# Performance work log

Hardware: AMD Instinct MI355X
Metric: run time of the kernel (lower is better)

## Reference

```python
import jax, jax.numpy as jnp
import numpy as np

C = 256          # in_channels == out_channels
L = 131072       # sequence length (multiple of BL)
BL = 64          # dilation == sliding-attention block length
CQ = C // 2      # q/k channels (r1=2)
CV = C // 2      # v channels (r2=2)
ALPHA = 1.0
EPS_IN = 1e-5    # InstanceNorm eps


def setup_inputs() -> dict:
    key = jax.random.key(0)
    ks = jax.random.split(key, 16)
    s = 0.05
    return {
        "x": jax.random.normal(ks[0], (1, C, L), jnp.float32),
        "f": jax.random.normal(ks[1], (1, C, L), jnp.float32),
        "mask": jnp.ones((1, 1, L), jnp.float32),
        # ConvFeedForward: Conv1d(C, C, 3, padding=BL, dilation=BL)
        "Wff": jax.random.normal(ks[2], (C, C, 3), jnp.float32) * s,
        "bff": jax.random.normal(ks[3], (C,), jnp.float32) * s,
        # AttLayer 1x1 convs
        "Wq": jax.random.normal(ks[4], (CQ, C), jnp.float32) * s,
        "bq": jax.random.normal(ks[5], (CQ,), jnp.float32) * s,
        "Wk": jax.random.normal(ks[6], (CQ, C), jnp.float32) * s,
        "bk": jax.random.normal(ks[7], (CQ,), jnp.float32) * s,
        "Wv": jax.random.normal(ks[8], (CV, C), jnp.float32) * s,
        "bv": jax.random.normal(ks[9], (CV,), jnp.float32) * s,
        "Wo": jax.random.normal(ks[10], (C, CV), jnp.float32) * s,
        "bo": jax.random.normal(ks[11], (C,), jnp.float32) * s,
        # AttModule.conv_1x1
        "Wc": jax.random.normal(ks[12], (C, C), jnp.float32) * s,
        "bc": jax.random.normal(ks[13], (C,), jnp.float32) * s,
    }


def _conv1x1(W, b, x):  # x: (B, Cin, L)
    return jnp.einsum('oc,bcl->bol', W, x) + b[None, :, None]


def _forward(x, f, mask, Wff, bff, Wq, bq, Wk, bk, Wv, bv, Wo, bo, Wc, bc):
    # --- ConvFeedForward: dilated conv + ReLU (same-length output) ---
    out = jax.lax.conv_general_dilated(
        x, Wff, window_strides=(1,), padding=[(BL, BL)], rhs_dilation=(BL,),
        dimension_numbers=('NCH', 'OIH', 'NCH')) + bff[None, :, None]
    out = jax.nn.relu(out)  # (1, C, L)

    # --- InstanceNorm1d (affine=False, biased var) ---
    mu = out.mean(axis=-1, keepdims=True)
    var = out.var(axis=-1, keepdims=True)
    xn = (out - mu) * jax.lax.rsqrt(var + EPS_IN)

    # --- AttLayer (sliding_att, decoder: value from f) ---
    q = _conv1x1(Wq, bq, xn)   # (1, CQ, L)
    k = _conv1x1(Wk, bk, xn)   # (1, CQ, L)
    v = _conv1x1(Wv, bv, f)    # (1, CV, L)

    nb = L // BL
    half = BL // 2
    pm = mask[:, 0:1, :]                         # (1,1,L) padding mask
    # pad halo of BL//2 zeros on each side of k, v, padding_mask
    kp = jnp.pad(k, ((0, 0), (0, 0), (half, half)))
    vp = jnp.pad(v, ((0, 0), (0, 0), (half, half)))
    mp = jnp.pad(pm, ((0, 0), (0, 0), (half, half)))
    # window index: block i sees [i*BL, i*BL + 2*BL) of the padded sequence
    idx = jnp.arange(nb)[:, None] * BL + jnp.arange(2 * BL)[None, :]  # (nb, 2BL)
    kw = kp[:, :, idx]   # (1, CQ, nb, 2BL)
    vw = vp[:, :, idx]   # (1, CV, nb, 2BL)
    mw = mp[:, 0, idx]   # (1, nb, 2BL)

    # window mask: query i attends keys [i, i+BL) within the 2BL window
    d = jnp.arange(2 * BL)[None, :] - jnp.arange(BL)[:, None]
    wm = ((d >= 0) & (d < BL)).astype(x.dtype)          # (BL, 2BL)
    fm = wm[None, None] * mw[:, :, None, :]             # (1, nb, BL, 2BL)

    qb = q.reshape(1, CQ, nb, BL)
    energy = jnp.einsum('bcnl,bcnm->bnlm', qb, kw) / np.sqrt(CQ).astype(x.dtype)
    att = jax.nn.softmax(energy + jnp.log(fm + 1e-6), axis=-1) * fm
    ov = jnp.einsum('bcnm,bnlm->bcnl', vw, att)         # (1, CV, nb, BL)
    oo = jnp.einsum('oc,bcnl->bonl', Wo, jax.nn.relu(ov)) + bo[None, :, None, None]
    att_out = oo.reshape(1, C, L) * pm                  # (1, C, L)

    # --- scaled residual + 1x1 conv + (dropout=identity) + masked residual ---
    h = ALPHA * att_out + out
    h = _conv1x1(Wc, bc, h)
    return (x + h) * mask


def reference(x, f, mask, Wff, bff, Wq, bq, Wk, bk, Wv, bv, Wo, bo, Wc, bc):
    return _forward(x, f, mask, Wff, bff, Wq, bq, Wk, bk, Wv, bv, Wo, bo, Wc, bc)
```

## Files before the change

### kernel.cpp

```cpp
#include <hip/hip_runtime.h>

#define L_LEN 131072
#define NB    2048
#define NT    1024

typedef unsigned short u16;
typedef __attribute__((ext_vector_type(4))) float f32x4;
typedef __attribute__((ext_vector_type(8))) short s16x8;
typedef __attribute__((ext_vector_type(4))) short s16x4;

#define WS_OUTT  0ull
#define WS_QT    67108864ull
#define WS_PSUM  100663296ull
#define WS_PSQ   101711872ull
#define WS_MEAN  102760448ull
#define WS_RSTD  102761472ull
#define WS_WFFB  102762496ull
#define WS_WQKB  103155712ull
#define WS_WVB   103286784ull
#define WS_WOB   103352320ull
#define WS_WCB   103417856ull
#define WS_BQKP  103548928ull

__device__ __forceinline__ u16 f2bf(float v){
  union { float f; unsigned u; } a; a.f = v;
  unsigned r = a.u + 0x7fffu + ((a.u >> 16) & 1u);
  return (u16)(r >> 16);
}
__device__ __forceinline__ float bf2f(u16 u){
  union { unsigned u; float f; } a; a.u = ((unsigned)u) << 16; return a.f;
}
__device__ __forceinline__ unsigned cvtpk(float a, float b){
  unsigned r;
  asm("v_cvt_pk_bf16_f32 %0, %1, %2" : "=v"(r) : "v"(a), "v"(b));
  return r;
}
__device__ __forceinline__ f32x4 mfma16(s16x8 a, s16x8 b, f32x4 c){
  return __builtin_amdgcn_mfma_f32_16x16x32_bf16(a, b, c, 0, 0, 0);
}
__device__ __forceinline__ s16x8 ld8(const void* p){ return *(const s16x8*)p; }

__global__ __launch_bounds__(256) void k_prep(
    const float* __restrict__ Wff, const float* __restrict__ Wv,
    const float* __restrict__ Wo,  const float* __restrict__ Wc,
    short* __restrict__ wffb, short* __restrict__ wvb,
    short* __restrict__ wob,  short* __restrict__ wcb)
{
  int i = blockIdx.x * 256 + threadIdx.x;
  if (i < 196608){
    int o = i / 768, kk = i % 768;
    int t = kk >> 8, c = kk & 255;
    wffb[i] = (short)f2bf(Wff[(o*256 + c)*3 + t]);
  } else if (i < 229376){ int j = i - 196608; wvb[j] = (short)f2bf(Wv[j]); }
  else if (i < 262144){ int j = i - 229376; wob[j] = (short)f2bf(Wo[j]); }
  else if (i < 327680){ int j = i - 262144; wcb[j] = (short)f2bf(Wc[j]); }
}

__global__ __launch_bounds__(512, 2) void k_conv(
    const float* __restrict__ x, const short* __restrict__ wffb,
    const float* __restrict__ bff, u16* __restrict__ outT,
    float* __restrict__ psum, float* __restrict__ psq)
{
  __shared__ u16 xs[2*256*40];
  const int wg = blockIdx.x, l0 = wg * 128;
  const int tid = threadIdx.x;
  const int w = tid >> 6, lane = tid & 63, p = lane & 15, g = lane >> 4;
  const int cl = tid >> 4, posq = tid & 15;

  {
    #pragma unroll
    for (int u = 0; u < 4; ++u){
      const int row = 64*u + 4*posq;
      const long gp = (long)l0 - 64 + row;
      f32x4 v = {0.f,0.f,0.f,0.f};
      if (gp >= 0 && gp + 4 <= L_LEN)
        v = *(const f32x4*)(x + (size_t)cl*L_LEN + gp);
      const unsigned r01 = cvtpk(v[0], v[1]);
      const unsigned r23 = cvtpk(v[2], v[3]);
      xs[(row+0)*40 + (cl ^ (8*(((row+0)>>2)&3)))] = (u16)(r01 & 0xffffu);
      xs[(row+1)*40 + (cl ^ (8*(((row+1)>>2)&3)))] = (u16)(r01 >> 16);
      xs[(row+2)*40 + (cl ^ (8*(((row+2)>>2)&3)))] = (u16)(r23 & 0xffffu);
      xs[(row+3)*40 + (cl ^ (8*(((row+3)>>2)&3)))] = (u16)(r23 >> 16);
    }
  }
  __syncthreads();

  f32x4 acc[2][8] = {};
  #pragma unroll 1
  for (int cg = 0; cg < 8; ++cg){
    const int cur = (cg & 1) * 10240;
    const int nxt = ((cg + 1) & 1) * 10240;
    f32x4 vv[4];
    const bool have = (cg < 7);
    if (have){
      #pragma unroll
      for (int u = 0; u < 4; ++u){
        const int row = 64*u + 4*posq;
        const long gp = (long)l0 - 64 + row;
        vv[u] = f32x4{0.f,0.f,0.f,0.f};
        if (gp >= 0 && gp + 4 <= L_LEN)
          vv[u] = *(const f32x4*)(x + (size_t)((cg+1)*32 + cl)*L_LEN + gp);
      }
    }
    #pragma unroll
    for (int t = 0; t < 3; ++t){
      s16x8 a0 = ld8(wffb + (size_t)(32*w +      p)*768 + t*256 + cg*32 + 8*g);
      s16x8 a1 = ld8(wffb + (size_t)(32*w + 16 + p)*768 + t*256 + cg*32 + 8*g);
      #pragma unroll
      for (int fn = 0; fn < 8; ++fn){
        const int row = 64*t + 16*fn + p;
        s16x8 b = ld8(&xs[cur + row*40 + ((8*g) ^ (8*((row>>2)&3)))]);
        acc[0][fn] = mfma16(a0, b, acc[0][fn]);
        acc[1][fn] = mfma16(a1, b, acc[1][fn]);
      }
    }
    if (have){
      #pragma unroll
      for (int u = 0; u < 4; ++u){
        const int row = 64*u + 4*posq;
        const unsigned r01 = cvtpk(vv[u][0], vv[u][1]);
        const unsigned r23 = cvtpk(vv[u][2], vv[u][3]);
        xs[nxt + (row+0)*40 + (cl ^ (8*(((row+0)>>2)&3)))] = (u16)(r01 & 0xffffu);
        xs[nxt + (row+1)*40 + (cl ^ (8*(((row+1)>>2)&3)))] = (u16)(r01 >> 16);
        xs[nxt + (row+2)*40 + (cl ^ (8*(((row+2)>>2)&3)))] = (u16)(r23 & 0xffffu);
        xs[nxt + (row+3)*40 + (cl ^ (8*(((row+3)>>2)&3)))] = (u16)(r23 >> 16);
      }
    }
    __syncthreads();
  }
  #pragma unroll
  for (int fm = 0; fm < 2; ++fm){
    const int o0 = 32*w + 16*fm + 4*g;
    float ssum[4] = {0,0,0,0}, ssq[4] = {0,0,0,0};
    #pragma unroll
    for (int fn = 0; fn < 8; ++fn){
      s16x4 pk;
      #pragma unroll
      for (int i = 0; i < 4; ++i){
        float val = fmaxf(acc[fm][fn][i] + bff[o0+i], 0.f);
        pk[i] = (short)f2bf(val);
        ssum[i] += val; ssq[i] += val*val;
      }
      *(s16x4*)(outT + (size_t)(l0 + 16*fn + p)*256 + o0) = pk;
    }
    #pragma unroll
    for (int i = 0; i < 4; ++i){
      float a = ssum[i], b = ssq[i];
      #pragma unroll
      for (int d = 1; d < 16; d <<= 1){ a += __shfl_xor(a, d, 16); b += __shfl_xor(b, d, 16); }
      if (p == 0){ psum[(size_t)(o0+i)*NT + wg] = a; psq[(size_t)(o0+i)*NT + wg] = b; }
    }
  }
}

__global__ __launch_bounds__(256) void k_stats(
    const float* __restrict__ psum, const float* __restrict__ psq,
    float* __restrict__ mean, float* __restrict__ rstd)
{
  __shared__ float ss[256], sq[256];
  const int ch = blockIdx.x, tid = threadIdx.x;
  float a = 0.f, b = 0.f;
  for (int j = tid; j < NT; j += 256){ a += psum[(size_t)ch*NT + j]; b += psq[(size_t)ch*NT + j]; }
  ss[tid] = a; sq[tid] = b;
  __syncthreads();
  for (int st = 128; st > 0; st >>= 1){
    if (tid < st){ ss[tid] += ss[tid+st]; sq[tid] += sq[tid+st]; }
    __syncthreads();
  }
  if (tid == 0){
    float m = ss[0] / (float)L_LEN;
    float v = sq[0] / (float)L_LEN - m*m;
    mean[ch] = m;
    rstd[ch] = rsqrtf(v + 1e-5f);
  }
}

__global__ __launch_bounds__(256) void k_adj(
    const float* __restrict__ Wq, const float* __restrict__ Wk,
    const float* __restrict__ bq, const float* __restrict__ bk,
    const float* __restrict__ mean, const float* __restrict__ rstd,
    short* __restrict__ wqkb, float* __restrict__ bqkp)
{
  __shared__ float red[256];
  const int o = blockIdx.x, c = threadIdx.x;
  const float* src = (o < 128) ? (Wq + (size_t)o*256) : (Wk + (size_t)(o-128)*256);
  const float bias = (o < 128) ? bq[o] : bk[o-128];
  float wv = src[c] * rstd[c];
  wqkb[o*256 + c] = (short)f2bf(wv);
  red[c] = wv * mean[c];
  __syncthreads();
  for (int st = 128; st > 0; st >>= 1){
    if (c < st) red[c] += red[c+st];
    __syncthreads();
  }
  if (c == 0) bqkp[o] = bias - red[0];
}

__global__ __launch_bounds__(512, 4) void k_v(
    const float* __restrict__ fin, const short* __restrict__ wvb,
    const float* __restrict__ bv, u16* __restrict__ vout)
{
  __shared__ u16 xs[2*128*40];
  const int wg = blockIdx.x, l0 = wg * 128;
  const int tid = threadIdx.x;
  const int w = tid >> 6, lane = tid & 63, p = lane & 15, g = lane >> 4;
  const int cl = tid >> 4, posq = tid & 15;

  {
    #pragma unroll
    for (int u = 0; u < 2; ++u){
      const int row = 8*posq + 4*u;
      f32x4 v = *(const f32x4*)(fin + (size_t)cl*L_LEN + l0 + row);
      const unsigned r01 = cvtpk(v[0], v[1]);
      const unsigned r23 = cvtpk(v[2], v[3]);
      xs[(row+0)*40 + (cl ^ (8*(((row+0)>>2)&3)))] = (u16)(r01 & 0xffffu);
      xs[(row+1)*40 + (cl ^ (8*(((row+1)>>2)&3)))] = (u16)(r01 >> 16);
      xs[(row+2)*40 + (cl ^ (8*(((row+2)>>2)&3)))] = (u16)(r23 & 0xffffu);
      xs[(row+3)*40 + (cl ^ (8*(((row+3)>>2)&3)))] = (u16)(r23 >> 16);
    }
  }
  __syncthreads();

  f32x4 acc[8] = {};
  #pragma unroll 1
  for (int cg = 0; cg < 8; ++cg){
    const int cur = (cg & 1) * 5120;
    const int nxt = ((cg + 1) & 1) * 5120;
    f32x4 vv[2];
    const bool have = (cg < 7);
    if (have){
      #pragma unroll
      for (int u = 0; u < 2; ++u){
        const int row = 8*posq + 4*u;
        vv[u] = *(const f32x4*)(fin + (size_t)((cg+1)*32 + cl)*L_LEN + l0 + row);
      }
    }
    s16x8 af = ld8(wvb + (size_t)(16*w + p)*256 + cg*32 + 8*g);
    #pragma unroll
    for (int fn = 0; fn < 8; ++fn){
      const int row = 16*fn + p;
      s16x8 b = ld8(&xs[cur + row*40 + ((8*g) ^ (8*((row>>2)&3)))]);
      acc[fn] = mfma16(af, b, acc[fn]);
    }
    if (have){
      #pragma unroll
      for (int u = 0; u < 2; ++u){
        const int row = 8*posq + 4*u;
        const unsigned r01 = cvtpk(vv[u][0], vv[u][1]);
        const unsigned r23 = cvtpk(vv[u][2], vv[u][3]);
        xs[nxt + (row+0)*40 + (cl ^ (8*(((row+0)>>2)&3)))] = (u16)(r01 & 0xffffu);
        xs[nxt + (row+1)*40 + (cl ^ (8*(((row+1)>>2)&3)))] = (u16)(r01 >> 16);
        xs[nxt + (row+2)*40 + (cl ^ (8*(((row+2)>>2)&3)))] = (u16)(r23 & 0xffffu);
        xs[nxt + (row+3)*40 + (cl ^ (8*(((row+3)>>2)&3)))] = (u16)(r23 >> 16);
      }
    }
    __syncthreads();
  }
  #pragma unroll
  for (int fn = 0; fn < 8; ++fn){
    #pragma unroll
    for (int i = 0; i < 4; ++i){
      const int cv = 16*w + 4*g + i;
      vout[(size_t)cv*L_LEN + l0 + 16*fn + p] = f2bf(acc[fn][i] + bv[cv]);
    }
  }
}

__global__ __launch_bounds__(512, 2) void k_qk(
    const u16* __restrict__ outT, const short* __restrict__ wqkb,
    const float* __restrict__ bqkp, u16* __restrict__ qT, u16* __restrict__ kT)
{
  extern __shared__ u16 tile[];
  const int wg = blockIdx.x, l0 = wg * 128;
  const int tid = threadIdx.x;
  const int w = tid >> 6, lane = tid & 63, p = lane & 15, g = lane >> 4;
  #pragma unroll
  for (int rep = 0; rep < 8; ++rep){
    const int idx = rep*512 + tid;
    const int r = idx >> 5, cc = idx & 31;
    s16x8 vput = ld8(outT + (size_t)(l0 + r)*256 + cc*8);
    *(s16x8*)(&tile[r*256 + ((cc*8) ^ ((r&7)<<3))]) = vput;
  }
  __syncthreads();
  f32x4 acc[2][8] = {};
  #pragma unroll
  for (int kk = 0; kk < 8; ++kk){
    s16x8 af[2];
    af[0] = ld8(wqkb + (size_t)(32*w +      p)*256 + 32*kk + 8*g);
    af[1] = ld8(wqkb + (size_t)(32*w + 16 + p)*256 + 32*kk + 8*g);
    #pragma unroll
    for (int fn = 0; fn < 8; ++fn){
      const int r = 16*fn + p;
      s16x8 b = ld8(&tile[r*256 + ((32*kk + 8*g) ^ ((r&7)<<3))]);
      acc[0][fn] = mfma16(af[0], b, acc[0][fn]);
      acc[1][fn] = mfma16(af[1], b, acc[1][fn]);
    }
  }
  #pragma unroll
  for (int fm = 0; fm < 2; ++fm){
    const int R0 = 32*w + 16*fm + 4*g;
    #pragma unroll
    for (int fn = 0; fn < 8; ++fn){
      s16x4 pk;
      #pragma unroll
      for (int i = 0; i < 4; ++i) pk[i] = (short)f2bf(acc[fm][fn][i] + bqkp[R0+i]);
      const size_t row = (size_t)(l0 + 16*fn + p);
      if (R0 < 128) *(s16x4*)(qT + row*128 + R0)       = pk;
      else          *(s16x4*)(kT + row*128 + R0 - 128) = pk;
    }
  }
}

__global__ __launch_bounds__(256, 4) void k_attn(
    const u16* __restrict__ qT, const u16* __restrict__ kT,
    const u16* __restrict__ vg, const short* __restrict__ wob,
    const float* __restrict__ bo, const float* __restrict__ mask,
    u16* __restrict__ outT)
{
  __shared__ u16 klds[16384];
  __shared__ float maskw[128];
  const int tid = threadIdx.x;
  const int w = tid >> 6, lane = tid & 63, p = lane & 15, g = lane >> 4;
  const int n = blockIdx.x, s = n * 64;
  const float SCALE = 0.08838834764831845f;

  #pragma unroll
  for (int rep = 0; rep < 8; ++rep){
    const int idx = rep*256 + tid;
    const int m = idx >> 4, cc = idx & 15;
    const int gpos = s - 32 + m;
    s16x8 vput = {};
    if (gpos >= 0 && gpos < L_LEN) vput = ld8(kT + (size_t)gpos*128 + cc*8);
    *(s16x8*)(&klds[m*128 + ((cc*8) ^ ((m&7)<<3))]) = vput;
  }
  if (tid < 128){
    const int gp = s - 32 + tid;
    maskw[tid] = (gp >= 0 && gp < L_LEN) ? mask[gp] : 0.f;
  }
  __syncthreads();

  f32x4 e[8] = {};
  #pragma unroll
  for (int kk = 0; kk < 4; ++kk){
    s16x8 aq = ld8(qT + (size_t)(s + 16*w + p)*128 + 32*kk + 8*g);
    #pragma unroll
    for (int fn = 0; fn < 8; ++fn){
      const int m = 16*fn + p;
      s16x8 b = ld8(&klds[m*128 + ((32*kk + 8*g) ^ ((m&7)<<3))]);
      e[fn] = mfma16(aq, b, e[fn]);
    }
  }
  float M[4] = {-1e30f,-1e30f,-1e30f,-1e30f};
  float S[4] = {0.f,0.f,0.f,0.f};
  #pragma unroll
  for (int fn = 0; fn < 8; ++fn){
    #pragma unroll
    for (int i = 0; i < 4; ++i){
      const int mm = 16*fn + p;
      const int l_ = 16*w + 4*g + i;
      const int d = mm - l_;
      const float fmv = (d >= 0 && d < 64) ? maskw[mm] : 0.f;
      const float z = e[fn][i]*SCALE + __logf(fmv + 1e-6f);
      e[fn][i] = z;
      M[i] = fmaxf(M[i], z);
    }
  }
  #pragma unroll
  for (int i = 0; i < 4; ++i){
    #pragma unroll
    for (int d = 1; d < 16; d <<= 1) M[i] = fmaxf(M[i], __shfl_xor(M[i], d, 16));
  }
  #pragma unroll
  for (int fn = 0; fn < 8; ++fn){
    #pragma unroll
    for (int i = 0; i < 4; ++i){
      const float pv = __expf(e[fn][i] - M[i]);
      e[fn][i] = pv;
      S[i] += pv;
    }
  }
  #pragma unroll
  for (int i = 0; i < 4; ++i){
    #pragma unroll
    for (int d = 1; d < 16; d <<= 1) S[i] += __shfl_xor(S[i], d, 16);
  }
  float rinv[4];
  #pragma unroll
  for (int i = 0; i < 4; ++i) rinv[i] = 1.f / S[i];
  __syncthreads();
  #pragma unroll
  for (int fn = 0; fn < 8; ++fn){
    #pragma unroll
    for (int i = 0; i < 4; ++i){
      const int mm = 16*fn + p;
      const int l_ = 16*w + 4*g + i;
      const int d = mm - l_;
      const float fmv = (d >= 0 && d < 64) ? maskw[mm] : 0.f;
      klds[l_*128 + (mm ^ ((l_&7)<<3))] = f2bf(e[fn][i] * rinv[i] * fmv);
    }
  }
  __syncthreads();

  f32x4 accp[2][4] = {};
  #pragma unroll
  for (int kk = 0; kk < 4; ++kk){
    int gp0 = s - 32 + 32*kk + 8*g;
    gp0 = max(0, min(gp0, L_LEN - 8));
    s16x8 a0 = ld8(vg + (size_t)(32*w +      p)*L_LEN + gp0);
    s16x8 a1 = ld8(vg + (size_t)(32*w + 16 + p)*L_LEN + gp0);
    #pragma unroll
    for (int fn = 0; fn < 4; ++fn){
      const int l_ = 16*fn + p;
      s16x8 b = ld8(&klds[l_*128 + ((32*kk + 8*g) ^ ((l_&7)<<3))]);
      accp[0][fn] = mfma16(a0, b, accp[0][fn]);
      accp[1][fn] = mfma16(a1, b, accp[1][fn]);
    }
  }
  #pragma unroll
  for (int fm = 0; fm < 2; ++fm){
    #pragma unroll
    for (int fn = 0; fn < 4; ++fn){
      const int l_ = 16*fn + p;
      s16x4 pk;
      #pragma unroll
      for (int i = 0; i < 4; ++i) pk[i] = (short)f2bf(fmaxf(accp[fm][fn][i], 0.f));
      const int cv0 = 32*w + 16*fm + 4*g;
      *(s16x4*)(&klds[8192 + l_*128 + (cv0 ^ ((l_&7)<<3))]) = pk;
    }
  }
  __syncthreads();

  f32x4 acco[4][4] = {};
  #pragma unroll
  for (int kk = 0; kk < 4; ++kk){
    s16x8 a[4];
    #pragma unroll
    for (int fm = 0; fm < 4; ++fm)
      a[fm] = ld8(wob + (size_t)(64*w + 16*fm + p)*128 + 32*kk + 8*g);
    #pragma unroll
    for (int fn = 0; fn < 4; ++fn){
      const int l_ = 16*fn + p;
      s16x8 b = ld8(&klds[8192 + l_*128 + ((32*kk + 8*g) ^ ((l_&7)<<3))]);
      #pragma unroll
      for (int fm = 0; fm < 4; ++fm) acco[fm][fn] = mfma16(a[fm], b, acco[fm][fn]);
    }
  }
  #pragma unroll
  for (int fm = 0; fm < 4; ++fm){
    const int o0 = 64*w + 16*fm + 4*g;
    #pragma unroll
    for (int fn = 0; fn < 4; ++fn){
      const int l_ = 16*fn + p;
      const float pml = maskw[32 + l_];
      u16* hp = outT + (size_t)(s + l_)*256 + o0;
      s16x4 res = *(const s16x4*)hp;
      s16x4 pk;
      #pragma unroll
      for (int i = 0; i < 4; ++i){
        float hv = (acco[fm][fn][i] + bo[o0+i]) * pml + bf2f((u16)res[i]);
        pk[i] = (short)f2bf(hv);
      }
      *(s16x4*)hp = pk;
    }
  }
}

__global__ __launch_bounds__(512, 2) void k_wc(
    const u16* __restrict__ hT, const short* __restrict__ wcb,
    const float* __restrict__ bc, const float* __restrict__ x,
    const float* __restrict__ mask, float* __restrict__ dout)
{
  extern __shared__ u16 tile[];
  const int wg = blockIdx.x, l0 = wg * 128;
  const int tid = threadIdx.x;
  const int w = tid >> 6, lane = tid & 63, p = lane & 15, g = lane >> 4;
  #pragma unroll
  for (int rep = 0; rep < 8; ++rep){
    const int idx = rep*512 + tid;
    const int r = idx >> 5, cc = idx & 31;
    s16x8 vput = ld8(hT + (size_t)(l0 + r)*256 + cc*8);
    *(s16x8*)(&tile[r*256 + ((cc*8) ^ ((r&7)<<3))]) = vput;
  }
  __syncthreads();
  f32x4 acc[2][8] = {};
  #pragma unroll
  for (int kk = 0; kk < 8; ++kk){
    s16x8 af[2];
    af[0] = ld8(wcb + (size_t)(32*w +      p)*256 + 32*kk + 8*g);
    af[1] = ld8(wcb + (size_t)(32*w + 16 + p)*256 + 32*kk + 8*g);
    #pragma unroll
    for (int fn = 0; fn < 8; ++fn){
      const int r = 16*fn + p;
      s16x8 b = ld8(&tile[r*256 + ((32*kk + 8*g) ^ ((r&7)<<3))]);
      acc[0][fn] = mfma16(af[0], b, acc[0][fn]);
      acc[1][fn] = mfma16(af[1], b, acc[1][fn]);
    }
  }
  #pragma unroll
  for (int fm = 0; fm < 2; ++fm){
    const int o0 = 32*w + 16*fm + 4*g;
    #pragma unroll
    for (int fn = 0; fn < 8; ++fn){
      const int pos = l0 + 16*fn + p;
      const float mk = mask[pos];
      #pragma unroll
      for (int i = 0; i < 4; ++i){
        const size_t idx = (size_t)(o0+i)*L_LEN + pos;
        dout[idx] = (x[idx] + acc[fm][fn][i] + bc[o0+i]) * mk;
      }
    }
  }
}

extern "C" void kernel_launch(void* const* d_in, const int* in_sizes, int n_in,
                              void* d_out, int out_size, void* d_ws, size_t ws_size,
                              hipStream_t stream)
{
  (void)in_sizes; (void)n_in; (void)out_size; (void)ws_size;
  const float* x    = (const float*)d_in[0];
  const float* f    = (const float*)d_in[1];
  const float* mask = (const float*)d_in[2];
  const float* Wff  = (const float*)d_in[3];
  const float* bff  = (const float*)d_in[4];
  const float* Wq   = (const float*)d_in[5];
  const float* bq   = (const float*)d_in[6];
  const float* Wk   = (const float*)d_in[7];
  const float* bk   = (const float*)d_in[8];
  const float* Wv   = (const float*)d_in[9];
  const float* bv   = (const float*)d_in[10];
  const float* Wo   = (const float*)d_in[11];
  const float* bo   = (const float*)d_in[12];
  const float* Wc   = (const float*)d_in[13];
  const float* bc   = (const float*)d_in[14];

  char* ws = (char*)d_ws;
  u16*   outT = (u16*)(ws + WS_OUTT);
  u16*   qT   = (u16*)(ws + WS_QT);
  float* psum = (float*)(ws + WS_PSUM);
  float* psq  = (float*)(ws + WS_PSQ);
  float* mean = (float*)(ws + WS_MEAN);
  float* rstd = (float*)(ws + WS_RSTD);
  short* wffb = (short*)(ws + WS_WFFB);
  short* wqkb = (short*)(ws + WS_WQKB);
  short* wvb  = (short*)(ws + WS_WVB);
  short* wob  = (short*)(ws + WS_WOB);
  short* wcb  = (short*)(ws + WS_WCB);
  float* bqkp = (float*)(ws + WS_BQKP);

  u16* vbuf = (u16*)d_out;
  u16* ktb  = (u16*)((char*)d_out + 33554432);

  (void)hipFuncSetAttribute((const void*)k_qk,
                            hipFuncAttributeMaxDynamicSharedMemorySize, 65536);
  (void)hipFuncSetAttribute((const void*)k_wc,
                            hipFuncAttributeMaxDynamicSharedMemorySize, 65536);

  k_prep <<<1280, 256, 0, stream>>>(Wff, Wv, Wo, Wc, wffb, wvb, wob, wcb);
  k_conv <<<NT,   512, 0, stream>>>(x, wffb, bff, outT, psum, psq);
  k_stats<<<256,  256, 0, stream>>>(psum, psq, mean, rstd);
  k_adj  <<<256,  256, 0, stream>>>(Wq, Wk, bq, bk, mean, rstd, wqkb, bqkp);
  k_v    <<<NT,   512, 0, stream>>>(f, wvb, bv, vbuf);
  k_qk   <<<NT,   512, 65536, stream>>>(outT, wqkb, bqkp, qT, ktb);
  k_attn <<<NB,   256, 0, stream>>>(qT, ktb, vbuf, wob, bo, mask, outT);
  k_wc   <<<NT,   512, 65536, stream>>>(outT, wcb, bc, x, mask, (float*)d_out);
}
```

Before: 357.1 us.

## Restructure dilated conv: stream weights via LDS, load activations directly to registers

Reworks the dilated-conv kernel so that each wave owns 16 output positions across all 256 output channels. Weight slices are staged into double-buffered LDS with global_load_lds, and the x values are loaded straight into registers and packed to bf16. This replaces the old scheme that converted x tiles through LDS and read weights from global. It also remaps block indices, raises occupancy to 4 blocks per SM, and reduces per-channel stats through LDS across waves. The cost is 24 sync iterations and strided scalar x loads (8 channels per lane, each a separate row).

```diff
diff --git a/kernel.cpp b/kernel.cpp
--- a/kernel.cpp
+++ b/kernel.cpp
@@ -39,6 +39,11 @@
   return __builtin_amdgcn_mfma_f32_16x16x32_bf16(a, b, c, 0, 0, 0);
 }
 __device__ __forceinline__ s16x8 ld8(const void* p){ return *(const s16x8*)p; }
+__device__ __forceinline__ void gl_lds16(const void* g, void* l){
+  __builtin_amdgcn_global_load_lds(
+      (const __attribute__((address_space(1))) unsigned int*)g,
+      (__attribute__((address_space(3))) unsigned int*)l, 16, 0, 0);
+}
 
 __global__ __launch_bounds__(256) void k_prep(
     const float* __restrict__ Wff, const float* __restrict__ Wv,
@@ -56,100 +61,108 @@
   else if (i < 327680){ int j = i - 262144; wcb[j] = (short)f2bf(Wc[j]); }
 }
 
-__global__ __launch_bounds__(512, 2) void k_conv(
+__global__ __launch_bounds__(512, 4) void k_conv(
     const float* __restrict__ x, const short* __restrict__ wffb,
     const float* __restrict__ bff, u16* __restrict__ outT,
     float* __restrict__ psum, float* __restrict__ psq)
 {
-  __shared__ u16 xs[2*256*40];
-  const int wg = blockIdx.x, l0 = wg * 128;
+  __shared__ u16 wlds[2*8192];
+  const int bid = blockIdx.x;
+  const int wg = (bid & 7) * 128 + (bid >> 3);
+  const int l0 = wg * 128;
   const int tid = threadIdx.x;
   const int w = tid >> 6, lane = tid & 63, p = lane & 15, g = lane >> 4;
-  const int cl = tid >> 4, posq = tid & 15;
-
-  {
-    #pragma unroll
-    for (int u = 0; u < 4; ++u){
-      const int row = 64*u + 4*posq;
-      const long gp = (long)l0 - 64 + row;
-      f32x4 v = {0.f,0.f,0.f,0.f};
-      if (gp >= 0 && gp + 4 <= L_LEN)
-        v = *(const f32x4*)(x + (size_t)cl*L_LEN + gp);
-      const unsigned r01 = cvtpk(v[0], v[1]);
-      const unsigned r23 = cvtpk(v[2], v[3]);
-      xs[(row+0)*40 + (cl ^ (8*(((row+0)>>2)&3)))] = (u16)(r01 & 0xffffu);
-      xs[(row+1)*40 + (cl ^ (8*(((row+1)>>2)&3)))] = (u16)(r01 >> 16);
-      xs[(row+2)*40 + (cl ^ (8*(((row+2)>>2)&3)))] = (u16)(r23 & 0xffffu);
-      xs[(row+3)*40 + (cl ^ (8*(((row+3)>>2)&3)))] = (u16)(r23 >> 16);
-    }
-  }
-  __syncthreads();
-
-  f32x4 acc[2][8] = {};
+
+  auto stage = [&](int it, int buf){
+    const int t = it >> 3, kk = it & 7;
+    const int kbase = t*256 + kk*32;
+    #pragma unroll
+    for (int j = 0; j < 2; ++j){
+      const int och = 32*w + 16*j + (lane >> 2);
+      const int srcblk = (lane & 3) ^ ((lane >> 3) & 3);
+      const short* src = wffb + (size_t)och*768 + kbase + srcblk*8;
+      u16* dst = &wlds[buf*8192 + (32*w + 16*j)*32];
+      gl_lds16(src, dst);
+    }
+  };
+  auto loadx = [&](int it, float* r){
+    const int t = it >> 3, kk = it & 7;
+    const int pa = l0 + 16*w + p + 64*t - 64;
+    const int pac = min(max(pa, 0), L_LEN - 1);
+    const bool ok = (pa >= 0) && (pa < L_LEN);
+    #pragma unroll
+    for (int j = 0; j < 8; ++j){
+      const int c = kk*32 + 8*g + j;
+      float v = x[(size_t)c*L_LEN + pac];
+      r[j] = ok ? v : 0.f;
+    }
+  };
+  auto pack8 = [&](const float* r) -> s16x8 {
+    union { unsigned u[4]; s16x8 v; } t;
+    t.u[0] = cvtpk(r[0], r[1]); t.u[1] = cvtpk(r[2], r[3]);
+    t.u[2] = cvtpk(r[4], r[5]); t.u[3] = cvtpk(r[6], r[7]);
+    return t.v;
+  };
+
+  float r[8];
+  loadx(0, r);
+  stage(0, 0);
+  __syncthreads();
+  s16x8 a_cur = pack8(r), a_nxt;
+
+  f32x4 acc[16] = {};
+  const int rb = p*32 + ((g ^ ((p >> 1) & 3)) * 8);
   #pragma unroll 1
-  for (int cg = 0; cg < 8; ++cg){
-    const int cur = (cg & 1) * 10240;
-    const int nxt = ((cg + 1) & 1) * 10240;
-    f32x4 vv[4];
-    const bool have = (cg < 7);
-    if (have){
-      #pragma unroll
-      for (int u = 0; u < 4; ++u){
-        const int row = 64*u + 4*posq;
-        const long gp = (long)l0 - 64 + row;
-        vv[u] = f32x4{0.f,0.f,0.f,0.f};
-        if (gp >= 0 && gp + 4 <= L_LEN)
-          vv[u] = *(const f32x4*)(x + (size_t)((cg+1)*32 + cl)*L_LEN + gp);
+  for (int it = 0; it < 24; ++it){
+    const int cur = it & 1;
+    if (it < 23){ stage(it + 1, cur ^ 1); loadx(it + 1, r); }
+    #pragma unroll
+    for (int fn = 0; fn < 16; ++fn){
+      s16x8 bw = ld8(&wlds[cur*8192 + rb + fn*512]);
+      acc[fn] = mfma16(bw, a_cur, acc[fn]);
+    }
+    if (it < 23) a_nxt = pack8(r);
+    __syncthreads();
+    a_cur = a_nxt;
+  }
+
+  float* sred = (float*)wlds;
+  const int pos = l0 + 16*w + p;
+  #pragma unroll
+  for (int fn = 0; fn < 16; ++fn){
+    const int och0 = 16*fn + 4*g;
+    s16x4 pk;
+    float sv[4], qv[4];
+    #pragma unroll
+    for (int i = 0; i < 4; ++i){
+      float val = fmaxf(acc[fn][i] + bff[och0 + i], 0.f);
+      pk[i] = (short)f2bf(val);
+      sv[i] = val; qv[i] = val*val;
+    }
+    *(s16x4*)(outT + (size_t)pos*256 + och0) = pk;
+    #pragma unroll
+    for (int i = 0; i < 4; ++i){
+      #pragma unroll
+      for (int d = 1; d < 16; d <<= 1){
+        sv[i] += __shfl_xor(sv[i], d, 16);
+        qv[i] += __shfl_xor(qv[i], d, 16);
       }
-    }
-    #pragma unroll
-    for (int t = 0; t < 3; ++t){
-      s16x8 a0 = ld8(wffb + (size_t)(32*w +      p)*768 + t*256 + cg*32 + 8*g);
-      s16x8 a1 = ld8(wffb + (size_t)(32*w + 16 + p)*768 + t*256 + cg*32 + 8*g);
-      #pragma unroll
-      for (int fn = 0; fn < 8; ++fn){
-        const int row = 64*t + 16*fn + p;
-        s16x8 b = ld8(&xs[cur + row*40 + ((8*g) ^ (8*((row>>2)&3)))]);
-        acc[0][fn] = mfma16(a0, b, acc[0][fn]);
-        acc[1][fn] = mfma16(a1, b, acc[1][fn]);
+      if (p == 0){
+        sred[(w*256 + och0 + i)*2 + 0] = sv[i];
+        sred[(w*256 + och0 + i)*2 + 1] = qv[i];
       }
     }
-    if (have){
-      #pragma unroll
-      for (int u = 0; u < 4; ++u){
-        const int row = 64*u + 4*posq;
-        const unsigned r01 = cvtpk(vv[u][0], vv[u][1]);
-        const unsigned r23 = cvtpk(vv[u][2], vv[u][3]);
-        xs[nxt + (row+0)*40 + (cl ^ (8*(((row+0)>>2)&3)))] = (u16)(r01 & 0xffffu);
-        xs[nxt + (row+1)*40 + (cl ^ (8*(((row+1)>>2)&3)))] = (u16)(r01 >> 16);
-        xs[nxt + (row+2)*40 + (cl ^ (8*(((row+2)>>2)&3)))] = (u16)(r23 & 0xffffu);
-        xs[nxt + (row+3)*40 + (cl ^ (8*(((row+3)>>2)&3)))] = (u16)(r23 >> 16);
-      }
-    }
-    __syncthreads();
-  }
-  #pragma unroll
-  for (int fm = 0; fm < 2; ++fm){
-    const int o0 = 32*w + 16*fm + 4*g;
-    float ssum[4] = {0,0,0,0}, ssq[4] = {0,0,0,0};
-    #pragma unroll
-    for (int fn = 0; fn < 8; ++fn){
-      s16x4 pk;
-      #pragma unroll
-      for (int i = 0; i < 4; ++i){
-        float val = fmaxf(acc[fm][fn][i] + bff[o0+i], 0.f);
-        pk[i] = (short)f2bf(val);
-        ssum[i] += val; ssq[i] += val*val;
-      }
-      *(s16x4*)(outT + (size_t)(l0 + 16*fn + p)*256 + o0) = pk;
-    }
-    #pragma unroll
-    for (int i = 0; i < 4; ++i){
-      float a = ssum[i], b = ssq[i];
-      #pragma unroll
-      for (int d = 1; d < 16; d <<= 1){ a += __shfl_xor(a, d, 16); b += __shfl_xor(b, d, 16); }
-      if (p == 0){ psum[(size_t)(o0+i)*NT + wg] = a; psq[(size_t)(o0+i)*NT + wg] = b; }
-    }
+  }
+  __syncthreads();
+  if (tid < 256){
+    float a = 0.f, b = 0.f;
+    #pragma unroll
+    for (int ww = 0; ww < 8; ++ww){
+      a += sred[(ww*256 + tid)*2 + 0];
+      b += sred[(ww*256 + tid)*2 + 1];
+    }
+    psum[(size_t)tid*NT + wg] = a;
+    psq [(size_t)tid*NT + wg] = b;
   }
 }
 
```

Result: slower. 380.0 us (+6.4%).

## Fold Wo projection into final Wc conv via precomputed Wc·Wo product

Applied to the files above, without the earlier changes.

Precomputes Wc·Wo (and Wc·bo) once in a new fold kernel, so the attention kernel writes only the relu'd attention values (128 channels) into the q buffer instead of running the Wo GEMM and doing a read-modify-write on the 256-channel residual buffer. The final 1x1 conv kernel then runs two GEMMs (Wc on the conv output and WcWo on the attention values) and applies the mask to the second term. This removes a GEMM and a 256-channel read+write pass from the attention stage, at the cost of an extra K=128 GEMM and input load in the last kernel. Rounding the folded weight to bf16 changes the numerics slightly.

```diff
diff --git a/kernel.cpp b/kernel.cpp
--- a/kernel.cpp
+++ b/kernel.cpp
@@ -18,9 +18,10 @@
 #define WS_WFFB  102762496ull
 #define WS_WQKB  103155712ull
 #define WS_WVB   103286784ull
-#define WS_WOB   103352320ull
+#define WS_WCCOB 103352320ull
 #define WS_WCB   103417856ull
 #define WS_BQKP  103548928ull
+#define WS_WCBO  103549952ull
 
 __device__ __forceinline__ u16 f2bf(float v){
   union { float f; unsigned u; } a; a.f = v;
@@ -42,9 +43,8 @@
 
 __global__ __launch_bounds__(256) void k_prep(
     const float* __restrict__ Wff, const float* __restrict__ Wv,
-    const float* __restrict__ Wo,  const float* __restrict__ Wc,
-    short* __restrict__ wffb, short* __restrict__ wvb,
-    short* __restrict__ wob,  short* __restrict__ wcb)
+    const float* __restrict__ Wc,
+    short* __restrict__ wffb, short* __restrict__ wvb, short* __restrict__ wcb)
 {
   int i = blockIdx.x * 256 + threadIdx.x;
   if (i < 196608){
@@ -52,8 +52,23 @@
     int t = kk >> 8, c = kk & 255;
     wffb[i] = (short)f2bf(Wff[(o*256 + c)*3 + t]);
   } else if (i < 229376){ int j = i - 196608; wvb[j] = (short)f2bf(Wv[j]); }
-  else if (i < 262144){ int j = i - 229376; wob[j] = (short)f2bf(Wo[j]); }
-  else if (i < 327680){ int j = i - 262144; wcb[j] = (short)f2bf(Wc[j]); }
+  else if (i < 294912){ int j = i - 229376; wcb[j] = (short)f2bf(Wc[j]); }
+}
+
+__global__ __launch_bounds__(128) void k_fold(
+    const float* __restrict__ Wc, const float* __restrict__ Wo,
+    const float* __restrict__ bo,
+    short* __restrict__ wccob, float* __restrict__ wcbo)
+{
+  const int o = blockIdx.x, j = threadIdx.x;
+  float s = 0.f;
+  for (int c = 0; c < 256; ++c) s += Wc[o*256 + c] * Wo[c*128 + j];
+  wccob[o*128 + j] = (short)f2bf(s);
+  if (j == 0){
+    float t = 0.f;
+    for (int c = 0; c < 256; ++c) t += Wc[o*256 + c] * bo[c];
+    wcbo[o] = t;
+  }
 }
 
 __global__ __launch_bounds__(512, 2) void k_conv(
@@ -312,10 +327,8 @@
 }
 
 __global__ __launch_bounds__(256, 4) void k_attn(
-    const u16* __restrict__ qT, const u16* __restrict__ kT,
-    const u16* __restrict__ vg, const short* __restrict__ wob,
-    const float* __restrict__ bo, const float* __restrict__ mask,
-    u16* __restrict__ outT)
+    u16* __restrict__ qT, const u16* __restrict__ kT,
+    const u16* __restrict__ vg, const float* __restrict__ mask)
 {
   __shared__ u16 klds[16384];
   __shared__ float maskw[128];
@@ -421,68 +434,36 @@
     #pragma unroll
     for (int fn = 0; fn < 4; ++fn){
       const int l_ = 16*fn + p;
+      const int cv0 = 32*w + 16*fm + 4*g;
       s16x4 pk;
       #pragma unroll
       for (int i = 0; i < 4; ++i) pk[i] = (short)f2bf(fmaxf(accp[fm][fn][i], 0.f));
-      const int cv0 = 32*w + 16*fm + 4*g;
-      *(s16x4*)(&klds[8192 + l_*128 + (cv0 ^ ((l_&7)<<3))]) = pk;
-    }
-  }
-  __syncthreads();
-
-  f32x4 acco[4][4] = {};
-  #pragma unroll
-  for (int kk = 0; kk < 4; ++kk){
-    s16x8 a[4];
-    #pragma unroll
-    for (int fm = 0; fm < 4; ++fm)
-      a[fm] = ld8(wob + (size_t)(64*w + 16*fm + p)*128 + 32*kk + 8*g);
-    #pragma unroll
-    for (int fn = 0; fn < 4; ++fn){
-      const int l_ = 16*fn + p;
-      s16x8 b = ld8(&klds[8192 + l_*128 + ((32*kk + 8*g) ^ ((l_&7)<<3))]);
-      #pragma unroll
-      for (int fm = 0; fm < 4; ++fm) acco[fm][fn] = mfma16(a[fm], b, acco[fm][fn]);
-    }
-  }
-  #pragma unroll
-  for (int fm = 0; fm < 4; ++fm){
-    const int o0 = 64*w + 16*fm + 4*g;
-    #pragma unroll
-    for (int fn = 0; fn < 4; ++fn){
-      const int l_ = 16*fn + p;
-      const float pml = maskw[32 + l_];
-      u16* hp = outT + (size_t)(s + l_)*256 + o0;
-      s16x4 res = *(const s16x4*)hp;
-      s16x4 pk;
-      #pragma unroll
-      for (int i = 0; i < 4; ++i){
-        float hv = (acco[fm][fn][i] + bo[o0+i]) * pml + bf2f((u16)res[i]);
-        pk[i] = (short)f2bf(hv);
-      }
-      *(s16x4*)hp = pk;
+      *(s16x4*)(qT + (size_t)(s + l_)*128 + cv0) = pk;
     }
   }
 }
 
 __global__ __launch_bounds__(512, 2) void k_wc(
-    const u16* __restrict__ hT, const short* __restrict__ wcb,
-    const float* __restrict__ bc, const float* __restrict__ x,
-    const float* __restrict__ mask, float* __restrict__ dout)
+    const u16* __restrict__ outT, const u16* __restrict__ rovT,
+    const short* __restrict__ wcb, const short* __restrict__ wccob,
+    const float* __restrict__ bc, const float* __restrict__ wcbo,
+    const float* __restrict__ x, const float* __restrict__ mask,
+    float* __restrict__ dout)
 {
   extern __shared__ u16 tile[];
   const int wg = blockIdx.x, l0 = wg * 128;
   const int tid = threadIdx.x;
   const int w = tid >> 6, lane = tid & 63, p = lane & 15, g = lane >> 4;
+
   #pragma unroll
   for (int rep = 0; rep < 8; ++rep){
     const int idx = rep*512 + tid;
     const int r = idx >> 5, cc = idx & 31;
-    s16x8 vput = ld8(hT + (size_t)(l0 + r)*256 + cc*8);
+    s16x8 vput = ld8(outT + (size_t)(l0 + r)*256 + cc*8);
     *(s16x8*)(&tile[r*256 + ((cc*8) ^ ((r&7)<<3))]) = vput;
   }
   __syncthreads();
-  f32x4 acc[2][8] = {};
+  f32x4 acc_a[2][8] = {};
   #pragma unroll
   for (int kk = 0; kk < 8; ++kk){
     s16x8 af[2];
@@ -492,10 +473,35 @@
     for (int fn = 0; fn < 8; ++fn){
       const int r = 16*fn + p;
       s16x8 b = ld8(&tile[r*256 + ((32*kk + 8*g) ^ ((r&7)<<3))]);
-      acc[0][fn] = mfma16(af[0], b, acc[0][fn]);
-      acc[1][fn] = mfma16(af[1], b, acc[1][fn]);
-    }
-  }
+      acc_a[0][fn] = mfma16(af[0], b, acc_a[0][fn]);
+      acc_a[1][fn] = mfma16(af[1], b, acc_a[1][fn]);
+    }
+  }
+  __syncthreads();
+
+  #pragma unroll
+  for (int rep = 0; rep < 4; ++rep){
+    const int idx = rep*512 + tid;
+    const int r = idx >> 4, cc = idx & 15;
+    s16x8 vput = ld8(rovT + (size_t)(l0 + r)*128 + cc*8);
+    *(s16x8*)(&tile[r*128 + ((cc*8) ^ ((r&7)<<3))]) = vput;
+  }
+  __syncthreads();
+  f32x4 acc_b[2][8] = {};
+  #pragma unroll
+  for (int kk = 0; kk < 4; ++kk){
+    s16x8 af[2];
+    af[0] = ld8(wccob + (size_t)(32*w +      p)*128 + 32*kk + 8*g);
+    af[1] = ld8(wccob + (size_t)(32*w + 16 + p)*128 + 32*kk + 8*g);
+    #pragma unroll
+    for (int fn = 0; fn < 8; ++fn){
+      const int r = 16*fn + p;
+      s16x8 b = ld8(&tile[r*128 + ((32*kk + 8*g) ^ ((r&7)<<3))]);
+      acc_b[0][fn] = mfma16(af[0], b, acc_b[0][fn]);
+      acc_b[1][fn] = mfma16(af[1], b, acc_b[1][fn]);
+    }
+  }
+
   #pragma unroll
   for (int fm = 0; fm < 2; ++fm){
     const int o0 = 32*w + 16*fm + 4*g;
@@ -506,7 +512,9 @@
       #pragma unroll
       for (int i = 0; i < 4; ++i){
         const size_t idx = (size_t)(o0+i)*L_LEN + pos;
-        dout[idx] = (x[idx] + acc[fm][fn][i] + bc[o0+i]) * mk;
+        const float y = acc_a[fm][fn][i] + bc[o0+i]
+                      + (acc_b[fm][fn][i] + wcbo[o0+i]) * mk;
+        dout[idx] = (x[idx] + y) * mk;
       }
     }
   }
@@ -534,18 +542,19 @@
   const float* bc   = (const float*)d_in[14];
 
   char* ws = (char*)d_ws;
-  u16*   outT = (u16*)(ws + WS_OUTT);
-  u16*   qT   = (u16*)(ws + WS_QT);
-  float* psum = (float*)(ws + WS_PSUM);
-  float* psq  = (float*)(ws + WS_PSQ);
-  float* mean = (float*)(ws + WS_MEAN);
-  float* rstd = (float*)(ws + WS_RSTD);
-  short* wffb = (short*)(ws + WS_WFFB);
-  short* wqkb = (short*)(ws + WS_WQKB);
-  short* wvb  = (short*)(ws + WS_WVB);
-  short* wob  = (short*)(ws + WS_WOB);
-  short* wcb  = (short*)(ws + WS_WCB);
-  float* bqkp = (float*)(ws + WS_BQKP);
+  u16*   outT  = (u16*)(ws + WS_OUTT);
+  u16*   qT    = (u16*)(ws + WS_QT);
+  float* psum  = (float*)(ws + WS_PSUM);
+  float* psq   = (float*)(ws + WS_PSQ);
+  float* mean  = (float*)(ws + WS_MEAN);
+  float* rstd  = (float*)(ws + WS_RSTD);
+  short* wffb  = (short*)(ws + WS_WFFB);
+  short* wqkb  = (short*)(ws + WS_WQKB);
+  short* wvb   = (short*)(ws + WS_WVB);
+  short* wccob = (short*)(ws + WS_WCCOB);
+  short* wcb   = (short*)(ws + WS_WCB);
+  float* bqkp  = (float*)(ws + WS_BQKP);
+  float* wcbo  = (float*)(ws + WS_WCBO);
 
   u16* vbuf = (u16*)d_out;
   u16* ktb  = (u16*)((char*)d_out + 33554432);
@@ -555,12 +564,14 @@
   (void)hipFuncSetAttribute((const void*)k_wc,
                             hipFuncAttributeMaxDynamicSharedMemorySize, 65536);
 
-  k_prep <<<1280, 256, 0, stream>>>(Wff, Wv, Wo, Wc, wffb, wvb, wob, wcb);
+  k_prep <<<1152, 256, 0, stream>>>(Wff, Wv, Wc, wffb, wvb, wcb);
+  k_fold <<<256,  128, 0, stream>>>(Wc, Wo, bo, wccob, wcbo);
   k_conv <<<NT,   512, 0, stream>>>(x, wffb, bff, outT, psum, psq);
   k_stats<<<256,  256, 0, stream>>>(psum, psq, mean, rstd);
   k_adj  <<<256,  256, 0, stream>>>(Wq, Wk, bq, bk, mean, rstd, wqkb, bqkp);
   k_v    <<<NT,   512, 0, stream>>>(f, wvb, bv, vbuf);
   k_qk   <<<NT,   512, 65536, stream>>>(outT, wqkb, bqkp, qT, ktb);
-  k_attn <<<NB,   256, 0, stream>>>(qT, ktb, vbuf, wob, bo, mask, outT);
-  k_wc   <<<NT,   512, 65536, stream>>>(outT, wcb, bc, x, mask, (float*)d_out);
-}
+  k_attn <<<NB,   256, 0, stream>>>(qT, ktb, vbuf, mask);
+  k_wc   <<<NT,   512, 65536, stream>>>(outT, qT, wcb, wccob, bc, wcbo, x, mask,
+                                        (float*)d_out);
+}
```

After: 411.0 us. +15.1%, slower.
